# Performance work log

Measured on AMD Instinct MI355X. Metric: run time of the kernel, lower is better.

## Reference

```python
import jax, jax.numpy as jnp
import numpy as np

OUT_FEATURES = 8192
IN_FEATURES = 4096  # d
CODEBOOK_SIZE = 16  # 2**bits, bits=4
BATCH = 32


def setup_inputs() -> dict:
    key = jax.random.key(0)
    k_x, k_idx, k_cb, k_r, k_b = jax.random.split(key, 5)
    x = jax.random.normal(k_x, (BATCH, IN_FEATURES), dtype=jnp.float32)
    indices = jax.random.randint(k_idx, (OUT_FEATURES, IN_FEATURES), 0, CODEBOOK_SIZE, dtype=jnp.int32)
    codebook = jax.random.normal(k_cb, (CODEBOOK_SIZE,), dtype=jnp.float32)
    # rotation matrix from the quantizer (orthogonal in the real impl; random here,
    # scaled for numerical stability)
    rotation_matrix = jax.random.normal(k_r, (IN_FEATURES, IN_FEATURES), dtype=jnp.float32) / np.sqrt(IN_FEATURES).astype(np.float32)
    bias = jax.random.normal(k_b, (OUT_FEATURES,), dtype=jnp.float32)
    return {"x": x, "indices": indices, "codebook": codebook,
            "rotation_matrix": rotation_matrix, "bias": bias}


def reference(x, indices, codebook, rotation_matrix, bias):
    # Dequantize: gather per-element codewords, then rotate back to weight space.
    # quantize was idx = Q(R @ w_row)  =>  w_row \approx R^T @ codebook[idx]
    codes = codebook[indices]                      # [O, D] gather
    weight = jnp.matmul(codes, rotation_matrix)    # [O, D]  (== (R^T @ c) per row)
    # F.linear(x, W, b) = x @ W^T + b
    return jnp.matmul(x, weight.T) + bias          # [B, O]
```

## Files before the change

kernel.cpp:

```cpp
#include <hip/hip_runtime.h>


#define IN_F 4096
#define OUT_F 8192
#define BATCH 32
#define TSa 136

typedef short bf16x8s __attribute__((ext_vector_type(8)));
typedef float f32x4 __attribute__((ext_vector_type(4)));
typedef int   i32x4 __attribute__((ext_vector_type(4)));

__device__ float y_buf[BATCH * IN_F];

__device__ __forceinline__ unsigned short f2bf(float f) {
    union { float f; unsigned int u; } v; v.f = f;
    unsigned int u = v.u;
    return (unsigned short)((u + 0x7fffu + ((u >> 16) & 1u)) >> 16);
}

__device__ __forceinline__ void load8_nt(f32x4* dst, const float* base, int coff) {
    #pragma unroll
    for (int jj = 0; jj < 8; ++jj)
        dst[jj] = __builtin_nontemporal_load((const f32x4*)(base + (size_t)jj * 8 * IN_F + coff));
}
__device__ __forceinline__ void load8i_nt(i32x4* dst, const int* base, int coff) {
    #pragma unroll
    for (int jj = 0; jj < 8; ++jj)
        dst[jj] = __builtin_nontemporal_load((const i32x4*)(base + (size_t)jj * 8 * IN_F + coff));
}
__device__ __forceinline__ void load4(f32x4* dst, const float* base, int coff) {
    #pragma unroll
    for (int ii = 0; ii < 4; ++ii)
        dst[ii] = *(const f32x4*)(base + (size_t)ii * 8 * IN_F + coff);
}
__device__ __forceinline__ void cvt8(unsigned short* lds, int lb, const f32x4* v) {
    #pragma unroll
    for (int jj = 0; jj < 8; ++jj) {
        ushort4 pv;
        pv.x = f2bf(v[jj].x); pv.y = f2bf(v[jj].y);
        pv.z = f2bf(v[jj].z); pv.w = f2bf(v[jj].w);
        *(ushort4*)&lds[lb + jj * 8 * TSa] = pv;
    }
}
__device__ __forceinline__ void cvt4(unsigned short* lds, int lb, const f32x4* v) {
    #pragma unroll
    for (int ii = 0; ii < 4; ++ii) {
        ushort4 pv;
        pv.x = f2bf(v[ii].x); pv.y = f2bf(v[ii].y);
        pv.z = f2bf(v[ii].z); pv.w = f2bf(v[ii].w);
        *(ushort4*)&lds[lb + ii * 8 * TSa] = pv;
    }
}
__device__ __forceinline__ void cvt_codes(unsigned short* lds, int lb, const i32x4* v,
                                          const unsigned int* cbp) {
    #pragma unroll
    for (int jj = 0; jj < 8; ++jj) {
        unsigned int key0 = (unsigned int)v[jj].x | ((unsigned int)v[jj].y << 4);
        unsigned int key1 = (unsigned int)v[jj].z | ((unsigned int)v[jj].w << 4);
        uint2 pv; pv.x = cbp[key0]; pv.y = cbp[key1];
        *(uint2*)&lds[lb + jj * 8 * TSa] = pv;
    }
}
__device__ __forceinline__ void mmstep(const unsigned short* B, const unsigned short* A,
                                       int bo, int ao, f32x4& acc0, f32x4& acc1) {
    #pragma unroll
    for (int ks = 0; ks < 4; ++ks) {
        bf16x8s bfr = *(const bf16x8s*)&B[bo + ks * 32];
        bf16x8s a0  = *(const bf16x8s*)&A[ao + ks * 32];
        bf16x8s a1  = *(const bf16x8s*)&A[ao + 16 * TSa + ks * 32];
        acc0 = __builtin_amdgcn_mfma_f32_16x16x32_bf16(a0, bfr, acc0, 0, 0, 0);
        acc1 = __builtin_amdgcn_mfma_f32_16x16x32_bf16(a1, bfr, acc1, 0, 0, 0);
    }
}

__global__ void __launch_bounds__(256) k0_zero() {
    int i = blockIdx.x * 256 + threadIdx.x;
    f32x4 z = {0.f, 0.f, 0.f, 0.f};
    ((f32x4*)y_buf)[i] = z;
}

__global__ void __launch_bounds__(256, 3) k1_xRT(const float* __restrict__ x,
                                                 const float* __restrict__ R,
                                                 const float* __restrict__ bias,
                                                 float* __restrict__ out) {
    __shared__ unsigned short Bl[2][64 * TSa];
    __shared__ unsigned short Al[2][32 * TSa];

    const int tid  = threadIdx.x;
    const int jt   = blockIdx.x & 63;
    const int kq   = blockIdx.x >> 6;
    const int j0   = jt * 64;
    const int kb   = kq * 512;
    const int wave = tid >> 6, lane = tid & 63;
    const int n = lane & 15, quad = lane >> 4;
    const int r0 = tid >> 5, c4 = tid & 31;

    const float* rbase = R + (size_t)(j0 + r0) * IN_F + kb + c4 * 4;
    const float* xbase = x + (size_t)r0 * IN_F + kb + c4 * 4;
    const int lb = r0 * TSa + c4 * 4;
    const int bo = (wave * 16 + n) * TSa + quad * 8;
    const int ao = n * TSa + quad * 8;

    f32x4 rvA[8], rvB[8], xvA[4], xvB[4];
    load8_nt(rvA, rbase, 0);
    load4(xvA, xbase, 0);

    {
        int e = (blockIdx.x * 256 + tid) * 2;
        float2 bv;
        bv.x = bias[e & (OUT_F - 1)];
        bv.y = bias[(e + 1) & (OUT_F - 1)];
        *(float2*)(out + e) = bv;
    }

    f32x4 acc0 = {0.f, 0.f, 0.f, 0.f};
    f32x4 acc1 = {0.f, 0.f, 0.f, 0.f};

    load8_nt(rvB, rbase, 128); load4(xvB, xbase, 128);
    cvt8(Bl[0], lb, rvA); cvt4(Al[0], lb, xvA);
    __syncthreads();
    mmstep(Bl[0], Al[0], bo, ao, acc0, acc1);

    load8_nt(rvA, rbase, 256); load4(xvA, xbase, 256);
    cvt8(Bl[1], lb, rvB); cvt4(Al[1], lb, xvB);
    __syncthreads();
    mmstep(Bl[1], Al[1], bo, ao, acc0, acc1);

    load8_nt(rvB, rbase, 384); load4(xvB, xbase, 384);
    cvt8(Bl[0], lb, rvA); cvt4(Al[0], lb, xvA);
    __syncthreads();
    mmstep(Bl[0], Al[0], bo, ao, acc0, acc1);

    cvt8(Bl[1], lb, rvB); cvt4(Al[1], lb, xvB);
    __syncthreads();
    mmstep(Bl[1], Al[1], bo, ao, acc0, acc1);

    const int jcol = j0 + wave * 16 + n;
    #pragma unroll
    for (int r = 0; r < 4; ++r) {
        int br = quad * 4 + r;
        atomicAdd(&y_buf[br * IN_F + jcol], acc0[r]);
        atomicAdd(&y_buf[(br + 16) * IN_F + jcol], acc1[r]);
    }
}

__global__ void __launch_bounds__(256, 3) k2_out(const int* __restrict__ idx,
                                                 const float* __restrict__ cb,
                                                 float* __restrict__ out) {
    __shared__ unsigned short Bl[2][64 * TSa];
    __shared__ unsigned short Al[2][32 * TSa];
    __shared__ unsigned int cbp[256];

    const int tid = threadIdx.x;
    const int ot = blockIdx.x & 127;
    const int kq = blockIdx.x >> 7;
    const int o0 = ot * 64;
    const int kb = kq * 512;
    const int wave = tid >> 6, lane = tid & 63;
    const int n = lane & 15, quad = lane >> 4;
    const int r0 = tid >> 5, c4 = tid & 31;

    const int*   ibase = idx + (size_t)(o0 + r0) * IN_F + kb + c4 * 4;
    const float* ybase = y_buf + (size_t)r0 * IN_F + kb + c4 * 4;
    const int lb = r0 * TSa + c4 * 4;
    const int bo = (wave * 16 + n) * TSa + quad * 8;
    const int ao = n * TSa + quad * 8;

    i32x4 ivA[8], ivB[8];
    f32x4 fvA[4], fvB[4];
    load8i_nt(ivA, ibase, 0);
    load4(fvA, ybase, 0);
    {
        unsigned int lo = f2bf(cb[tid & 15]);
        unsigned int hi = f2bf(cb[tid >> 4]);
        cbp[tid] = lo | (hi << 16);
    }
    load8i_nt(ivB, ibase, 128); load4(fvB, ybase, 128);
    __syncthreads();

    f32x4 acc0 = {0.f, 0.f, 0.f, 0.f};
    f32x4 acc1 = {0.f, 0.f, 0.f, 0.f};

    cvt_codes(Bl[0], lb, ivA, cbp); cvt4(Al[0], lb, fvA);
    __syncthreads();
    mmstep(Bl[0], Al[0], bo, ao, acc0, acc1);

    load8i_nt(ivA, ibase, 256); load4(fvA, ybase, 256);
    cvt_codes(Bl[1], lb, ivB, cbp); cvt4(Al[1], lb, fvB);
    __syncthreads();
    mmstep(Bl[1], Al[1], bo, ao, acc0, acc1);

    load8i_nt(ivB, ibase, 384); load4(fvB, ybase, 384);
    cvt_codes(Bl[0], lb, ivA, cbp); cvt4(Al[0], lb, fvA);
    __syncthreads();
    mmstep(Bl[0], Al[0], bo, ao, acc0, acc1);

    cvt_codes(Bl[1], lb, ivB, cbp); cvt4(Al[1], lb, fvB);
    __syncthreads();
    mmstep(Bl[1], Al[1], bo, ao, acc0, acc1);

    const int ocol = o0 + wave * 16 + n;
    #pragma unroll
    for (int r = 0; r < 4; ++r) {
        int br = quad * 4 + r;
        atomicAdd(&out[(size_t)br * OUT_F + ocol], acc0[r]);
        atomicAdd(&out[(size_t)(br + 16) * OUT_F + ocol], acc1[r]);
    }
}

extern "C" void kernel_launch(void* const* d_in, const int* in_sizes, int n_in,
                              void* d_out, int out_size, void* d_ws, size_t ws_size,
                              hipStream_t stream) {
    (void)in_sizes; (void)n_in; (void)out_size; (void)d_ws; (void)ws_size;
    const float* x       = (const float*)d_in[0];
    const int*   indices = (const int*)d_in[1];
    const float* cb      = (const float*)d_in[2];
    const float* R       = (const float*)d_in[3];
    const float* bias    = (const float*)d_in[4];
    float* out  = (float*)d_out;

    k0_zero<<<dim3(128),  dim3(256), 0, stream>>>();
    k1_xRT<<<dim3(512),  dim3(256), 0, stream>>>(x, R, bias, out);
    k2_out<<<dim3(1024), dim3(256), 0, stream>>>(indices, cb, out);
}
```

Before: 236.5 us.

## Widen LDS stores to 16-byte, prefetch deeper, and double K-split per block in k2

Each thread now loads two adjacent float4/int4 vectors (8 elements) per row and writes them to LDS as one 16-byte packed bf16 store, replacing 8-byte stores. The next tile's global loads are issued right after the LDS conversion, before the barrier, so memory latency overlaps the barrier and the MFMA step. k2 processes 1024 of K per block over 8 pipelined steps with half the grid, which halves the output atomics at the cost of fewer blocks in flight.

```diff
diff --git a/kernel.cpp b/kernel.cpp
--- a/kernel.cpp
+++ b/kernel.cpp
@@ -7,6 +7,7 @@
 #define TSa 136
 
 typedef short bf16x8s __attribute__((ext_vector_type(8)));
+typedef unsigned short u16x8 __attribute__((ext_vector_type(8)));
 typedef float f32x4 __attribute__((ext_vector_type(4)));
 typedef int   i32x4 __attribute__((ext_vector_type(4)));
 
@@ -18,47 +19,55 @@
     return (unsigned short)((u + 0x7fffu + ((u >> 16) & 1u)) >> 16);
 }
 
-__device__ __forceinline__ void load8_nt(f32x4* dst, const float* base, int coff) {
-    #pragma unroll
-    for (int jj = 0; jj < 8; ++jj)
-        dst[jj] = __builtin_nontemporal_load((const f32x4*)(base + (size_t)jj * 8 * IN_F + coff));
-}
-__device__ __forceinline__ void load8i_nt(i32x4* dst, const int* base, int coff) {
-    #pragma unroll
-    for (int jj = 0; jj < 8; ++jj)
-        dst[jj] = __builtin_nontemporal_load((const i32x4*)(base + (size_t)jj * 8 * IN_F + coff));
-}
-__device__ __forceinline__ void load4(f32x4* dst, const float* base, int coff) {
-    #pragma unroll
-    for (int ii = 0; ii < 4; ++ii)
-        dst[ii] = *(const f32x4*)(base + (size_t)ii * 8 * IN_F + coff);
-}
-__device__ __forceinline__ void cvt8(unsigned short* lds, int lb, const f32x4* v) {
-    #pragma unroll
-    for (int jj = 0; jj < 8; ++jj) {
-        ushort4 pv;
-        pv.x = f2bf(v[jj].x); pv.y = f2bf(v[jj].y);
-        pv.z = f2bf(v[jj].z); pv.w = f2bf(v[jj].w);
-        *(ushort4*)&lds[lb + jj * 8 * TSa] = pv;
-    }
-}
-__device__ __forceinline__ void cvt4(unsigned short* lds, int lb, const f32x4* v) {
-    #pragma unroll
-    for (int ii = 0; ii < 4; ++ii) {
-        ushort4 pv;
-        pv.x = f2bf(v[ii].x); pv.y = f2bf(v[ii].y);
-        pv.z = f2bf(v[ii].z); pv.w = f2bf(v[ii].w);
-        *(ushort4*)&lds[lb + ii * 8 * TSa] = pv;
-    }
-}
-__device__ __forceinline__ void cvt_codes(unsigned short* lds, int lb, const i32x4* v,
-                                          const unsigned int* cbp) {
-    #pragma unroll
-    for (int jj = 0; jj < 8; ++jj) {
-        unsigned int key0 = (unsigned int)v[jj].x | ((unsigned int)v[jj].y << 4);
-        unsigned int key1 = (unsigned int)v[jj].z | ((unsigned int)v[jj].w << 4);
-        uint2 pv; pv.x = cbp[key0]; pv.y = cbp[key1];
-        *(uint2*)&lds[lb + jj * 8 * TSa] = pv;
+
+__device__ __forceinline__ void loadB_nt(f32x4* dst, const float* base, int coff) {
+    #pragma unroll
+    for (int u = 0; u < 4; ++u) {
+        dst[2*u]   = __builtin_nontemporal_load((const f32x4*)(base + (size_t)u * 16 * IN_F + coff));
+        dst[2*u+1] = __builtin_nontemporal_load((const f32x4*)(base + (size_t)u * 16 * IN_F + coff + 4));
+    }
+}
+__device__ __forceinline__ void loadBi_nt(i32x4* dst, const int* base, int coff) {
+    #pragma unroll
+    for (int u = 0; u < 4; ++u) {
+        dst[2*u]   = __builtin_nontemporal_load((const i32x4*)(base + (size_t)u * 16 * IN_F + coff));
+        dst[2*u+1] = __builtin_nontemporal_load((const i32x4*)(base + (size_t)u * 16 * IN_F + coff + 4));
+    }
+}
+__device__ __forceinline__ void loadA(f32x4* dst, const float* base, int coff) {
+    #pragma unroll
+    for (int u = 0; u < 2; ++u) {
+        dst[2*u]   = *(const f32x4*)(base + (size_t)u * 16 * IN_F + coff);
+        dst[2*u+1] = *(const f32x4*)(base + (size_t)u * 16 * IN_F + coff + 4);
+    }
+}
+__device__ __forceinline__ u16x8 pack8(const f32x4 a, const f32x4 b) {
+    u16x8 pv;
+    pv[0] = f2bf(a.x); pv[1] = f2bf(a.y); pv[2] = f2bf(a.z); pv[3] = f2bf(a.w);
+    pv[4] = f2bf(b.x); pv[5] = f2bf(b.y); pv[6] = f2bf(b.z); pv[7] = f2bf(b.w);
+    return pv;
+}
+__device__ __forceinline__ void cvtB16(unsigned short* lds, int lb, const f32x4* v) {
+    #pragma unroll
+    for (int u = 0; u < 4; ++u)
+        *(u16x8*)&lds[lb + u * 16 * TSa] = pack8(v[2*u], v[2*u+1]);
+}
+__device__ __forceinline__ void cvtA16(unsigned short* lds, int lb, const f32x4* v) {
+    #pragma unroll
+    for (int u = 0; u < 2; ++u)
+        *(u16x8*)&lds[lb + u * 16 * TSa] = pack8(v[2*u], v[2*u+1]);
+}
+__device__ __forceinline__ void cvtC16(unsigned short* lds, int lb, const i32x4* v,
+                                       const unsigned int* cbp) {
+    #pragma unroll
+    for (int u = 0; u < 4; ++u) {
+        const i32x4 a = v[2*u], b = v[2*u+1];
+        uint4 pv;
+        pv.x = cbp[(unsigned int)a.x | ((unsigned int)a.y << 4)];
+        pv.y = cbp[(unsigned int)a.z | ((unsigned int)a.w << 4)];
+        pv.z = cbp[(unsigned int)b.x | ((unsigned int)b.y << 4)];
+        pv.w = cbp[(unsigned int)b.z | ((unsigned int)b.w << 4)];
+        *(uint4*)&lds[lb + u * 16 * TSa] = pv;
     }
 }
 __device__ __forceinline__ void mmstep(const unsigned short* B, const unsigned short* A,
@@ -93,17 +102,16 @@
     const int kb   = kq * 512;
     const int wave = tid >> 6, lane = tid & 63;
     const int n = lane & 15, quad = lane >> 4;
-    const int r0 = tid >> 5, c4 = tid & 31;
-
-    const float* rbase = R + (size_t)(j0 + r0) * IN_F + kb + c4 * 4;
-    const float* xbase = x + (size_t)r0 * IN_F + kb + c4 * 4;
-    const int lb = r0 * TSa + c4 * 4;
+    const int rg = tid >> 4, c8 = tid & 15;
+
+    const float* rbase = R + (size_t)(j0 + rg) * IN_F + kb + c8 * 8;
+    const float* xbase = x + (size_t)rg * IN_F + kb + c8 * 8;
+    const int lb = rg * TSa + c8 * 8;
     const int bo = (wave * 16 + n) * TSa + quad * 8;
     const int ao = n * TSa + quad * 8;
 
     f32x4 rvA[8], rvB[8], xvA[4], xvB[4];
-    load8_nt(rvA, rbase, 0);
-    load4(xvA, xbase, 0);
+    loadB_nt(rvA, rbase, 0);   loadA(xvA, xbase, 0);
 
     {
         int e = (blockIdx.x * 256 + tid) * 2;
@@ -112,26 +120,26 @@
         bv.y = bias[(e + 1) & (OUT_F - 1)];
         *(float2*)(out + e) = bv;
     }
+    loadB_nt(rvB, rbase, 128); loadA(xvB, xbase, 128);
 
     f32x4 acc0 = {0.f, 0.f, 0.f, 0.f};
     f32x4 acc1 = {0.f, 0.f, 0.f, 0.f};
 
-    load8_nt(rvB, rbase, 128); load4(xvB, xbase, 128);
-    cvt8(Bl[0], lb, rvA); cvt4(Al[0], lb, xvA);
+    cvtB16(Bl[0], lb, rvA); cvtA16(Al[0], lb, xvA);
+    loadB_nt(rvA, rbase, 256); loadA(xvA, xbase, 256);
     __syncthreads();
     mmstep(Bl[0], Al[0], bo, ao, acc0, acc1);
 
-    load8_nt(rvA, rbase, 256); load4(xvA, xbase, 256);
-    cvt8(Bl[1], lb, rvB); cvt4(Al[1], lb, xvB);
+    cvtB16(Bl[1], lb, rvB); cvtA16(Al[1], lb, xvB);
+    loadB_nt(rvB, rbase, 384); loadA(xvB, xbase, 384);
     __syncthreads();
     mmstep(Bl[1], Al[1], bo, ao, acc0, acc1);
 
-    load8_nt(rvB, rbase, 384); load4(xvB, xbase, 384);
-    cvt8(Bl[0], lb, rvA); cvt4(Al[0], lb, xvA);
+    cvtB16(Bl[0], lb, rvA); cvtA16(Al[0], lb, xvA);
     __syncthreads();
     mmstep(Bl[0], Al[0], bo, ao, acc0, acc1);
 
-    cvt8(Bl[1], lb, rvB); cvt4(Al[1], lb, xvB);
+    cvtB16(Bl[1], lb, rvB); cvtA16(Al[1], lb, xvB);
     __syncthreads();
     mmstep(Bl[1], Al[1], bo, ao, acc0, acc1);
 
@@ -155,49 +163,46 @@
     const int ot = blockIdx.x & 127;
     const int kq = blockIdx.x >> 7;
     const int o0 = ot * 64;
-    const int kb = kq * 512;
+    const int kb = kq * 1024;
     const int wave = tid >> 6, lane = tid & 63;
     const int n = lane & 15, quad = lane >> 4;
-    const int r0 = tid >> 5, c4 = tid & 31;
-
-    const int*   ibase = idx + (size_t)(o0 + r0) * IN_F + kb + c4 * 4;
-    const float* ybase = y_buf + (size_t)r0 * IN_F + kb + c4 * 4;
-    const int lb = r0 * TSa + c4 * 4;
+    const int rg = tid >> 4, c8 = tid & 15;
+
+    const int*   ibase = idx + (size_t)(o0 + rg) * IN_F + kb + c8 * 8;
+    const float* ybase = y_buf + (size_t)rg * IN_F + kb + c8 * 8;
+    const int lb = rg * TSa + c8 * 8;
     const int bo = (wave * 16 + n) * TSa + quad * 8;
     const int ao = n * TSa + quad * 8;
 
     i32x4 ivA[8], ivB[8];
     f32x4 fvA[4], fvB[4];
-    load8i_nt(ivA, ibase, 0);
-    load4(fvA, ybase, 0);
+    loadBi_nt(ivA, ibase, 0);   loadA(fvA, ybase, 0);
     {
         unsigned int lo = f2bf(cb[tid & 15]);
         unsigned int hi = f2bf(cb[tid >> 4]);
         cbp[tid] = lo | (hi << 16);
     }
-    load8i_nt(ivB, ibase, 128); load4(fvB, ybase, 128);
+    loadBi_nt(ivB, ibase, 128); loadA(fvB, ybase, 128);
     __syncthreads();
 
     f32x4 acc0 = {0.f, 0.f, 0.f, 0.f};
     f32x4 acc1 = {0.f, 0.f, 0.f, 0.f};
 
-    cvt_codes(Bl[0], lb, ivA, cbp); cvt4(Al[0], lb, fvA);
-    __syncthreads();
-    mmstep(Bl[0], Al[0], bo, ao, acc0, acc1);
-
-    load8i_nt(ivA, ibase, 256); load4(fvA, ybase, 256);
-    cvt_codes(Bl[1], lb, ivB, cbp); cvt4(Al[1], lb, fvB);
-    __syncthreads();
-    mmstep(Bl[1], Al[1], bo, ao, acc0, acc1);
-
-    load8i_nt(ivB, ibase, 384); load4(fvB, ybase, 384);
-    cvt_codes(Bl[0], lb, ivA, cbp); cvt4(Al[0], lb, fvA);
-    __syncthreads();
-    mmstep(Bl[0], Al[0], bo, ao, acc0, acc1);
-
-    cvt_codes(Bl[1], lb, ivB, cbp); cvt4(Al[1], lb, fvB);
-    __syncthreads();
-    mmstep(Bl[1], Al[1], bo, ao, acc0, acc1);
+    #define K2_STEP(P, IV, FV, DOLOAD, NOFF)                          \
+        cvtC16(Bl[P], lb, IV, cbp); cvtA16(Al[P], lb, FV);            \
+        if (DOLOAD) { loadBi_nt(IV, ibase, NOFF); loadA(FV, ybase, NOFF); } \
+        __syncthreads();                                              \
+        mmstep(Bl[P], Al[P], bo, ao, acc0, acc1);
+
+    K2_STEP(0, ivA, fvA, 1, 256)
+    K2_STEP(1, ivB, fvB, 1, 384)
+    K2_STEP(0, ivA, fvA, 1, 512)
+    K2_STEP(1, ivB, fvB, 1, 640)
+    K2_STEP(0, ivA, fvA, 1, 768)
+    K2_STEP(1, ivB, fvB, 1, 896)
+    K2_STEP(0, ivA, fvA, 0, 0)
+    K2_STEP(1, ivB, fvB, 0, 0)
+    #undef K2_STEP
 
     const int ocol = o0 + wave * 16 + n;
     #pragma unroll
@@ -219,7 +224,7 @@
     const float* bias    = (const float*)d_in[4];
     float* out  = (float*)d_out;
 
-    k0_zero<<<dim3(128),  dim3(256), 0, stream>>>();
-    k1_xRT<<<dim3(512),  dim3(256), 0, stream>>>(x, R, bias, out);
-    k2_out<<<dim3(1024), dim3(256), 0, stream>>>(indices, cb, out);
-}
+    k0_zero<<<dim3(128), dim3(256), 0, stream>>>();
+    k1_xRT<<<dim3(512), dim3(256), 0, stream>>>(x, R, bias, out);
+    k2_out<<<dim3(512), dim3(256), 0, stream>>>(indices, cb, out);
+}
```

Measured after the change: 238.8 us. No clear change (+1.0%).
